# Kernel tuning notes

Measured on AMD Instinct MI355X. Metric: run time of the kernel, lower is better.

Reference implementation:

```python
import jax, jax.numpy as jnp
import numpy as np

N_USERS, N_MOVIES, H, E = 100000, 50000, 128, 1000000


def setup_inputs() -> dict:
    key = jax.random.key(0)
    k1, k2, k3, k4, k5, k6 = jax.random.split(key, 6)
    scale1 = 1.0 / np.sqrt(2 * H)  # torch Linear default-ish init scale
    scale2 = 1.0 / np.sqrt(H)
    return {
        "z_user": jax.random.normal(k1, (N_USERS, H), dtype=jnp.float32),
        "z_movie": jax.random.normal(k2, (N_MOVIES, H), dtype=jnp.float32),
        "row": jax.random.randint(k3, (E,), 0, N_USERS, dtype=jnp.int64) if jax.config.jax_enable_x64 else jax.random.randint(k3, (E,), 0, N_USERS, dtype=jnp.int32),
        "col": jax.random.randint(k4, (E,), 0, N_MOVIES, dtype=jnp.int32),
        "W1": jax.random.normal(k5, (H, 2 * H), dtype=jnp.float32) * scale1,
        "b1": jnp.zeros((H,), dtype=jnp.float32),
        "W2": jax.random.normal(k6, (1, H), dtype=jnp.float32) * scale2,
        "b2": jnp.zeros((1,), dtype=jnp.float32),
    }


def reference(z_user, z_movie, row, col, W1, b1, W2, b2):
    zu = z_user[row]            # [E, H] gather
    zm = z_movie[col]           # [E, H] gather
    z = jnp.concatenate([zu, zm], axis=-1)        # [E, 2H]
    h = jax.nn.relu(z @ W1.T + b1)                # [E, H]
    out = h @ W2.T + b2                           # [E, 1]
    return out.reshape(-1)
```

## Files before the change

kernel.cpp:

```cpp
#include <hip/hip_runtime.h>
#include <stdint.h>

typedef __attribute__((ext_vector_type(8))) short bf16x8;
typedef __attribute__((ext_vector_type(8))) char  char8;
typedef __attribute__((ext_vector_type(4))) float f32x4;
typedef __attribute__((ext_vector_type(4))) int   i32x4;

#define SU      (4.5f / 127.0f)
#define INV_SU  (127.0f / 4.5f)
#define MAGIC   12582912.0f

__device__ __forceinline__ unsigned short f2bf(float f) {
    uint32_t u = __builtin_bit_cast(uint32_t, f);
    uint32_t r = (u + 0x7FFFu + ((u >> 16) & 1u)) >> 16;
    return (unsigned short)r;
}

__device__ __forceinline__ bf16x8 cvt8(f32x4 a, f32x4 b) {
    bf16x8 v;
#pragma unroll
    for (int i = 0; i < 4; ++i) v[i] = (short)f2bf(a[i]);
#pragma unroll
    for (int i = 0; i < 4; ++i) v[4 + i] = (short)f2bf(b[i]);
    return v;
}

__device__ __forceinline__ unsigned swz256(int n, int kbyte) {
    return ((unsigned)(n * 256 + kbyte)) ^ (unsigned)((n & 7) << 4);
}

__global__ __launch_bounds__(256) void precompute_h1(
    const float* __restrict__ zu, const float* __restrict__ zm,
    const float* __restrict__ W1, const float* __restrict__ b1,
    char* __restrict__ h1u8, char* __restrict__ h1m8,
    int Mu, int Mm, int bu)
{
    __shared__ __align__(16) char Bs[32768];
    const int tid  = threadIdx.x;
    const int wid  = tid >> 6;
    const int lane = tid & 63;
    const int g    = lane >> 4;
    const int lm   = lane & 15;

    const bool isU = (int)blockIdx.x < bu;
    const float* z = isU ? zu : zm;
    char* h1       = isU ? h1u8 : h1m8;
    const int M    = isU ? Mu : Mm;
    const int koff = isU ? 0 : 128;
    const int rbase = (isU ? blockIdx.x : blockIdx.x - bu) * 256 + wid * 64;

#pragma unroll
    for (int it = 0; it < 8; ++it) {
        int c  = it * 256 + tid;
        int n  = c >> 4;
        int kc = c & 15;
        const float* src = W1 + n * 256 + koff + kc * 8;
        f32x4 a = *reinterpret_cast<const f32x4*>(src);
        f32x4 b = *reinterpret_cast<const f32x4*>(src + 4);
        *reinterpret_cast<bf16x8*>(&Bs[swz256(n, kc * 16)]) = cvt8(a, b);
    }
    __syncthreads();

    float bs[8];
#pragma unroll
    for (int nt = 0; nt < 8; ++nt) bs[nt] = 0.5f * INV_SU * b1[nt * 16 + lm];

    f32x4 acc[4][8];
#pragma unroll
    for (int mt = 0; mt < 4; ++mt)
#pragma unroll
        for (int nt = 0; nt < 8; ++nt) acc[mt][nt] = f32x4{0.f, 0.f, 0.f, 0.f};

#pragma unroll
    for (int ks = 0; ks < 4; ++ks) {
        bf16x8 a[4];
#pragma unroll
        for (int mt = 0; mt < 4; ++mt) {
            int r = rbase + mt * 16 + lm;
            r = r < M ? r : M - 1;
            const float* p = z + (size_t)r * 128 + ks * 32 + g * 8;
            f32x4 x0 = *reinterpret_cast<const f32x4*>(p);
            f32x4 x1 = *reinterpret_cast<const f32x4*>(p + 4);
            a[mt] = cvt8(x0, x1);
        }
        const int kbyte = (ks * 32 + g * 8) * 2;
#pragma unroll
        for (int nt = 0; nt < 8; ++nt) {
            bf16x8 bfr = *reinterpret_cast<const bf16x8*>(&Bs[swz256(nt * 16 + lm, kbyte)]);
#pragma unroll
            for (int mt = 0; mt < 4; ++mt)
                acc[mt][nt] = __builtin_amdgcn_mfma_f32_16x16x32_bf16(
                    a[mt], bfr, acc[mt][nt], 0, 0, 0);
        }
    }

#pragma unroll
    for (int mt = 0; mt < 4; ++mt) {
#pragma unroll
        for (int r = 0; r < 4; ++r) {
            const int m = rbase + mt * 16 + g * 4 + r;
            if (m < M) {
                char* dst = h1 + (size_t)m * 128 + lm;
#pragma unroll
                for (int nt = 0; nt < 8; ++nt) {
                    float t = fmaf(acc[mt][nt][r], INV_SU, bs[nt]);
                    float c = fminf(127.f, fmaxf(-127.f, t));
                    float f = c + MAGIC;
                    dst[nt * 16] = (char)(__builtin_bit_cast(uint32_t, f) & 0xFFu);
                }
            }
        }
    }
}

__global__ __launch_bounds__(256) void edge_score(
    const char* __restrict__ h1u8, const char* __restrict__ h1m8,
    const int* __restrict__ row, const int* __restrict__ col,
    const float* __restrict__ W2, const float* __restrict__ b2,
    float* __restrict__ out, int nE)
{
    const int tid = blockIdx.x * 256 + threadIdx.x;
    const int g   = tid >> 4;
    const int l   = tid & 15;
    const int e0  = g * 8;
    if (e0 >= nE) return;

    float w2s[8];
    {
        f32x4 c0 = *reinterpret_cast<const f32x4*>(W2 + l * 8);
        f32x4 c1 = *reinterpret_cast<const f32x4*>(W2 + l * 8 + 4);
#pragma unroll
        for (int j = 0; j < 4; ++j) { w2s[j] = c0[j] * SU; w2s[4 + j] = c1[j] * SU; }
    }
    const float b2s = b2[0];

    int ridx[8], cidx[8];
    if (e0 + 8 <= nE) {
        i32x4 r0 = __builtin_nontemporal_load(reinterpret_cast<const i32x4*>(row + e0));
        i32x4 r1 = __builtin_nontemporal_load(reinterpret_cast<const i32x4*>(row + e0 + 4));
        i32x4 c0 = __builtin_nontemporal_load(reinterpret_cast<const i32x4*>(col + e0));
        i32x4 c1 = __builtin_nontemporal_load(reinterpret_cast<const i32x4*>(col + e0 + 4));
#pragma unroll
        for (int j = 0; j < 4; ++j) { ridx[j] = r0[j]; ridx[4 + j] = r1[j]; }
#pragma unroll
        for (int j = 0; j < 4; ++j) { cidx[j] = c0[j]; cidx[4 + j] = c1[j]; }
    } else {
#pragma unroll
        for (int j = 0; j < 8; ++j) {
            int e = e0 + j;
            e = e < nE ? e : nE - 1;
            ridx[j] = row[e];
            cidx[j] = col[e];
        }
    }

    char8 u[8], m[8];
#pragma unroll
    for (int j = 0; j < 8; ++j)
        u[j] = *reinterpret_cast<const char8*>(h1u8 + (size_t)ridx[j] * 128 + l * 8);
#pragma unroll
    for (int j = 0; j < 8; ++j)
        m[j] = *reinterpret_cast<const char8*>(h1m8 + (size_t)cidx[j] * 128 + l * 8);
    __builtin_amdgcn_sched_barrier(0);

    float s[8];
#pragma unroll
    for (int j = 0; j < 8; ++j) {
        float acc = 0.f;
#pragma unroll
        for (int q = 0; q < 8; ++q) {
            int su = (int)u[j][q] + (int)m[j][q];
            su = su > 0 ? su : 0;
            acc = fmaf((float)su, w2s[q], acc);
        }
        acc += __shfl_xor(acc, 1);
        acc += __shfl_xor(acc, 2);
        acc += __shfl_xor(acc, 4);
        acc += __shfl_xor(acc, 8);
        s[j] = acc + b2s;
    }

    float v = 0.f;
#pragma unroll
    for (int j = 0; j < 8; ++j) v = (l == j) ? s[j] : v;
    const int e = e0 + l;
    if (l < 8 && e < nE) __builtin_nontemporal_store(v, out + e);
}

__device__ __forceinline__ unsigned swzB(int n, int kbyte) {
    return ((unsigned)(n * 512 + kbyte)) ^ (unsigned)((n & 7) << 4);
}

__global__ __launch_bounds__(256, 2) void edge_mlp_fallback(
    const float* __restrict__ z_user, const float* __restrict__ z_movie,
    const int* __restrict__ row, const int* __restrict__ col,
    const float* __restrict__ W1, const float* __restrict__ b1,
    const float* __restrict__ W2, const float* __restrict__ b2,
    float* __restrict__ out, int nE, int ntiles)
{
    __shared__ __align__(16) char Bs[65536];
    const int tid  = threadIdx.x;
    const int wid  = tid >> 6;
    const int lane = tid & 63;
    const int g    = lane >> 4;
    const int lm   = lane & 15;

#pragma unroll
    for (int it = 0; it < 16; ++it) {
        int c  = it * 256 + tid;
        int n  = c >> 5;
        int kc = c & 31;
        const float* src = W1 + n * 256 + kc * 8;
        f32x4 a = *reinterpret_cast<const f32x4*>(src);
        f32x4 b = *reinterpret_cast<const f32x4*>(src + 4);
        *reinterpret_cast<bf16x8*>(&Bs[swzB(n, kc * 16)]) = cvt8(a, b);
    }
    __syncthreads();

    float b1v[8], w2v[8];
#pragma unroll
    for (int nt = 0; nt < 8; ++nt) {
        int n = nt * 16 + lm;
        b1v[nt] = b1[n];
        w2v[nt] = W2[n];
    }
    const float b2s = b2[0];

    for (int tile = blockIdx.x; tile < ntiles; tile += gridDim.x) {
        const int ebase = tile * 256 + wid * 64;
        int re[4], ce[4];
#pragma unroll
        for (int mt = 0; mt < 4; ++mt) {
            int e = ebase + mt * 16 + lm;
            e = e < nE ? e : nE - 1;
            re[mt] = row[e];
            ce[mt] = col[e];
        }
        f32x4 acc[4][8];
#pragma unroll
        for (int mt = 0; mt < 4; ++mt)
#pragma unroll
            for (int nt = 0; nt < 8; ++nt) acc[mt][nt] = f32x4{0.f, 0.f, 0.f, 0.f};
#pragma unroll
        for (int half = 0; half < 2; ++half) {
#pragma unroll
            for (int ks = 0; ks < 4; ++ks) {
                bf16x8 a[4];
#pragma unroll
                for (int mt = 0; mt < 4; ++mt) {
                    const float* p = (half ? z_movie + (size_t)ce[mt] * 128
                                           : z_user + (size_t)re[mt] * 128) + ks * 32 + g * 8;
                    f32x4 x0 = *reinterpret_cast<const f32x4*>(p);
                    f32x4 x1 = *reinterpret_cast<const f32x4*>(p + 4);
                    a[mt] = cvt8(x0, x1);
                }
                const int kbyte = (half * 128 + ks * 32 + g * 8) * 2;
#pragma unroll
                for (int nt = 0; nt < 8; ++nt) {
                    bf16x8 bfr = *reinterpret_cast<const bf16x8*>(&Bs[swzB(nt * 16 + lm, kbyte)]);
#pragma unroll
                    for (int mt = 0; mt < 4; ++mt)
                        acc[mt][nt] = __builtin_amdgcn_mfma_f32_16x16x32_bf16(
                            a[mt], bfr, acc[mt][nt], 0, 0, 0);
                }
            }
        }
#pragma unroll
        for (int mt = 0; mt < 4; ++mt) {
#pragma unroll
            for (int r = 0; r < 4; ++r) {
                float s = 0.f;
#pragma unroll
                for (int nt = 0; nt < 8; ++nt)
                    s += fmaxf(acc[mt][nt][r] + b1v[nt], 0.f) * w2v[nt];
                s += __shfl_xor(s, 8);
                s += __shfl_xor(s, 4);
                s += __shfl_xor(s, 2);
                s += __shfl_xor(s, 1);
                if (lm == 0) {
                    int e = ebase + mt * 16 + g * 4 + r;
                    if (e < nE) out[e] = s + b2s;
                }
            }
        }
    }
}

extern "C" void kernel_launch(void* const* d_in, const int* in_sizes, int n_in,
                              void* d_out, int out_size, void* d_ws, size_t ws_size,
                              hipStream_t stream) {
    const float* z_user  = (const float*)d_in[0];
    const float* z_movie = (const float*)d_in[1];
    const int*   row     = (const int*)d_in[2];
    const int*   col     = (const int*)d_in[3];
    const float* W1      = (const float*)d_in[4];
    const float* b1      = (const float*)d_in[5];
    const float* W2      = (const float*)d_in[6];
    const float* b2      = (const float*)d_in[7];
    float*       out     = (float*)d_out;

    const int nE = in_sizes[2];
    const int Mu = in_sizes[0] / 128;
    const int Mm = in_sizes[1] / 128;

    const size_t need = ((size_t)Mu + (size_t)Mm) * 128;

    if (ws_size >= need) {
        char* h1u8 = (char*)d_ws;
        char* h1m8 = h1u8 + (size_t)Mu * 128;

        const int bu = (Mu + 255) / 256;
        const int bm = (Mm + 255) / 256;
        precompute_h1<<<bu + bm, 256, 0, stream>>>(z_user, z_movie, W1, b1,
                                                   h1u8, h1m8, Mu, Mm, bu);

        const int nGroups = (nE + 7) / 8;
        const int blocks  = (nGroups * 16 + 255) / 256;
        edge_score<<<blocks, 256, 0, stream>>>(h1u8, h1m8, row, col,
                                               W2, b2, out, nE);
    } else {
        const int ntiles = (nE + 255) / 256;
        const int grid   = ntiles < 512 ? ntiles : 512;
        edge_mlp_fallback<<<grid, 256, 0, stream>>>(z_user, z_movie, row, col,
                                                    W1, b1, W2, b2, out, nE, ntiles);
    }
}
```

Baseline: 62.82 us.

## Stage node rows through padded LDS with coalesced loads in h1 precompute

The precompute kernel now loads each block's 128 rows of z with fully coalesced 16-byte loads, converts them to bf16, and stores them in padded shared memory. MFMA A-fragments are then read from LDS instead of strided global loads. Each block covers 128 rows instead of 256, which doubles the grid and halves the accumulators per wave. The int8 output stores become nontemporal. The cost is extra LDS use (about 35 KB more per block), which may lower occupancy, plus a synchronization before compute.

New measurement: 58.53 us. 6.8% less time.

```diff
diff --git a/kernel.cpp b/kernel.cpp
--- a/kernel.cpp
+++ b/kernel.cpp
@@ -2,6 +2,7 @@
 #include <stdint.h>
 
 typedef __attribute__((ext_vector_type(8))) short bf16x8;
+typedef __attribute__((ext_vector_type(4))) short bf16x4;
 typedef __attribute__((ext_vector_type(8))) char  char8;
 typedef __attribute__((ext_vector_type(4))) float f32x4;
 typedef __attribute__((ext_vector_type(4))) int   i32x4;
@@ -9,6 +10,7 @@
 #define SU      (4.5f / 127.0f)
 #define INV_SU  (127.0f / 4.5f)
 #define MAGIC   12582912.0f
+#define ZROWB   280
 
 __device__ __forceinline__ unsigned short f2bf(float f) {
     uint32_t u = __builtin_bit_cast(uint32_t, f);
@@ -22,6 +24,13 @@
     for (int i = 0; i < 4; ++i) v[i] = (short)f2bf(a[i]);
 #pragma unroll
     for (int i = 0; i < 4; ++i) v[4 + i] = (short)f2bf(b[i]);
+    return v;
+}
+
+__device__ __forceinline__ bf16x4 cvt4(f32x4 a) {
+    bf16x4 v;
+#pragma unroll
+    for (int i = 0; i < 4; ++i) v[i] = (short)f2bf(a[i]);
     return v;
 }
 
@@ -36,6 +45,7 @@
     int Mu, int Mm, int bu)
 {
     __shared__ __align__(16) char Bs[32768];
+    __shared__ __align__(16) char Zs[128 * ZROWB];
     const int tid  = threadIdx.x;
     const int wid  = tid >> 6;
     const int lane = tid & 63;
@@ -47,7 +57,8 @@
     char* h1       = isU ? h1u8 : h1m8;
     const int M    = isU ? Mu : Mm;
     const int koff = isU ? 0 : 128;
-    const int rbase = (isU ? blockIdx.x : blockIdx.x - bu) * 256 + wid * 64;
+    const int rbase0 = (isU ? blockIdx.x : blockIdx.x - bu) * 128;
+    const int rbase  = rbase0 + wid * 32;
 
 #pragma unroll
     for (int it = 0; it < 8; ++it) {
@@ -59,43 +70,55 @@
         f32x4 b = *reinterpret_cast<const f32x4*>(src + 4);
         *reinterpret_cast<bf16x8*>(&Bs[swz256(n, kc * 16)]) = cvt8(a, b);
     }
+
+#pragma unroll
+    for (int i = 0; i < 16; ++i) {
+        const int off  = i * 4096 + tid * 16;
+        const int frow = off >> 9;
+        const int cb   = off & 511;
+        int grow = rbase0 + frow;
+        grow = grow < M ? grow : M - 1;
+        f32x4 x = *reinterpret_cast<const f32x4*>(
+            reinterpret_cast<const char*>(z + (size_t)grow * 128) + cb);
+        *reinterpret_cast<bf16x4*>(&Zs[frow * ZROWB + (cb >> 1)]) = cvt4(x);
+    }
     __syncthreads();
 
     float bs[8];
 #pragma unroll
     for (int nt = 0; nt < 8; ++nt) bs[nt] = 0.5f * INV_SU * b1[nt * 16 + lm];
 
-    f32x4 acc[4][8];
-#pragma unroll
-    for (int mt = 0; mt < 4; ++mt)
+    f32x4 acc[2][8];
+#pragma unroll
+    for (int mt = 0; mt < 2; ++mt)
 #pragma unroll
         for (int nt = 0; nt < 8; ++nt) acc[mt][nt] = f32x4{0.f, 0.f, 0.f, 0.f};
 
 #pragma unroll
     for (int ks = 0; ks < 4; ++ks) {
-        bf16x8 a[4];
-#pragma unroll
-        for (int mt = 0; mt < 4; ++mt) {
-            int r = rbase + mt * 16 + lm;
-            r = r < M ? r : M - 1;
-            const float* p = z + (size_t)r * 128 + ks * 32 + g * 8;
-            f32x4 x0 = *reinterpret_cast<const f32x4*>(p);
-            f32x4 x1 = *reinterpret_cast<const f32x4*>(p + 4);
-            a[mt] = cvt8(x0, x1);
+        bf16x8 a[2];
+#pragma unroll
+        for (int mt = 0; mt < 2; ++mt) {
+            const int row = wid * 32 + mt * 16 + lm;
+            const char* p = &Zs[row * ZROWB + ks * 64 + g * 16];
+            bf16x4 lo = *reinterpret_cast<const bf16x4*>(p);
+            bf16x4 hi = *reinterpret_cast<const bf16x4*>(p + 8);
+#pragma unroll
+            for (int j = 0; j < 4; ++j) { a[mt][j] = lo[j]; a[mt][4 + j] = hi[j]; }
         }
         const int kbyte = (ks * 32 + g * 8) * 2;
 #pragma unroll
         for (int nt = 0; nt < 8; ++nt) {
             bf16x8 bfr = *reinterpret_cast<const bf16x8*>(&Bs[swz256(nt * 16 + lm, kbyte)]);
 #pragma unroll
-            for (int mt = 0; mt < 4; ++mt)
+            for (int mt = 0; mt < 2; ++mt)
                 acc[mt][nt] = __builtin_amdgcn_mfma_f32_16x16x32_bf16(
                     a[mt], bfr, acc[mt][nt], 0, 0, 0);
         }
     }
 
 #pragma unroll
-    for (int mt = 0; mt < 4; ++mt) {
+    for (int mt = 0; mt < 2; ++mt) {
 #pragma unroll
         for (int r = 0; r < 4; ++r) {
             const int m = rbase + mt * 16 + g * 4 + r;
@@ -106,7 +129,8 @@
                     float t = fmaf(acc[mt][nt][r], INV_SU, bs[nt]);
                     float c = fminf(127.f, fmaxf(-127.f, t));
                     float f = c + MAGIC;
-                    dst[nt * 16] = (char)(__builtin_bit_cast(uint32_t, f) & 0xFFu);
+                    __builtin_nontemporal_store(
+                        (char)(__builtin_bit_cast(uint32_t, f) & 0xFFu), dst + nt * 16);
                 }
             }
         }
@@ -309,8 +333,8 @@
         char* h1u8 = (char*)d_ws;
         char* h1m8 = h1u8 + (size_t)Mu * 128;
 
-        const int bu = (Mu + 255) / 256;
-        const int bm = (Mm + 255) / 256;
+        const int bu = (Mu + 127) / 128;
+        const int bm = (Mm + 127) / 128;
         precompute_h1<<<bu + bm, 256, 0, stream>>>(z_user, z_movie, W1, b1,
                                                    h1u8, h1m8, Mu, Mm, bu);
 
```
